# Kernel optimization log

Hardware: AMD Instinct MI355X
Metric: run time of the kernel (lower is better)

The kernel has to match this reference:

```python
import jax, jax.numpy as jnp
import numpy as np

D_MODEL, HEAD, B, S = 1024, 64, 4, 2048

def setup_inputs() -> dict:
    key = jax.random.key(0)
    ks = jax.random.split(key, 7)
    sc = 0.02
    return {
        "x": jax.random.normal(ks[0], (B, S, D_MODEL), dtype=jnp.float32),
        "w_q": jax.random.normal(ks[1], (D_MODEL, HEAD), dtype=jnp.float32) * sc,
        "b_q": jax.random.normal(ks[2], (HEAD,), dtype=jnp.float32) * sc,
        "w_k": jax.random.normal(ks[3], (D_MODEL, HEAD), dtype=jnp.float32) * sc,
        "b_k": jax.random.normal(ks[4], (HEAD,), dtype=jnp.float32) * sc,
        "w_v": jax.random.normal(ks[5], (D_MODEL, HEAD), dtype=jnp.float32) * sc,
        "b_v": jax.random.normal(ks[6], (HEAD,), dtype=jnp.float32) * sc,
    }

def reference(x, w_q, b_q, w_k, b_k, w_v, b_v):
    # q, k, v: [B, S, H]
    q = jnp.einsum('bsd,dh->bsh', x, w_q) + b_q
    k = jnp.einsum('bsd,dh->bsh', x, w_k) + b_k
    v = jnp.einsum('bsd,dh->bsh', x, w_v) + b_v
    head = k.shape[-1]
    # Source divides by (1/sqrt(d)) i.e. multiplies by sqrt(d) -- kept faithful.
    scores = jnp.einsum('bqh,bkh->bqk', q, k) * jnp.sqrt(jnp.float32(head))
    seq = x.shape[1]
    causal = jnp.tril(jnp.ones((seq, seq), dtype=bool))  # [S, S]
    scores = jnp.where(causal, scores, -jnp.inf)
    att = jax.nn.softmax(scores, axis=-1)
    # dropout is identity in eval / p=0
    return jnp.einsum('bqk,bkh->bqh', att, v)
```

## Files before the change

kernel.cpp:

```cpp
#include <hip/hip_runtime.h>
#include <math.h>

#define D_MODEL 1024
#define HEAD 64
#define BATCH 4
#define SEQ 2048
#define M_TOT (BATCH*SEQ)

typedef short short8 __attribute__((ext_vector_type(8)));
typedef float f32x4 __attribute__((ext_vector_type(4)));
typedef unsigned short ushort_t;

__device__ __forceinline__ unsigned short f2bf(float x) {
    union { float f; unsigned u; } v; v.f = x;
    unsigned r = (v.u + 0x7FFFu + ((v.u >> 16) & 1u)) >> 16;
    return (unsigned short)r;
}
__device__ __forceinline__ unsigned short f2bf_trunc(float x) {
    union { float f; unsigned u; } v; v.f = x;
    return (unsigned short)(v.u >> 16);
}
__device__ __forceinline__ float bf2f(unsigned short h) {
    union { unsigned u; float f; } v; v.u = ((unsigned)h) << 16;
    return v.f;
}

__global__ __launch_bounds__(256) void wsplit_kernel(
    const float* __restrict__ wq, const float* __restrict__ wk,
    const float* __restrict__ wv,
    ushort_t* __restrict__ Wfhi, ushort_t* __restrict__ Wflo)
{
    int tid = blockIdx.x * 256 + threadIdx.x;
    int l = tid & 63;
    int c = l & 15, g = l >> 4;
    int rest = tid >> 6;
    int nt = rest % 12, ks = rest / 12;
    const float* W = (nt < 4) ? wq : ((nt < 8) ? wk : wv);
    int colm = ((nt & 3) * 16) + c;
    short8 hi, lo;
#pragma unroll
    for (int e = 0; e < 8; ++e) {
        float v = W[(size_t)(32 * ks + 8 * g + e) * HEAD + colm];
        unsigned short h = f2bf_trunc(v);
        hi[e] = (short)h;
        lo[e] = (short)f2bf(v - bf2f(h));
    }
    *(short8*)&Wfhi[(size_t)tid * 8] = hi;
    *(short8*)&Wflo[(size_t)tid * 8] = lo;
}

#define KSLAB 128
#define XSTR 132

__global__ __launch_bounds__(256) void proj_kernel(
    const float* __restrict__ x,
    const ushort_t* __restrict__ Wfhi, const ushort_t* __restrict__ Wflo,
    const float* __restrict__ bq, const float* __restrict__ bk,
    const float* __restrict__ bv,
    ushort_t* __restrict__ Qhi, ushort_t* __restrict__ Qlo,
    float* __restrict__ Kw, ushort_t* __restrict__ Vt)
{
    __shared__ __align__(16) ushort_t xh_lds[2][16][XSTR];
    __shared__ __align__(16) ushort_t xl_lds[2][16][XSTR];
    __shared__ float eld[4][3][16][17];

    const int t = threadIdx.x;
    const int w = t >> 6;
    const int l = t & 63;
    const int c = l & 15, g = l >> 4;
    const int m0 = blockIdx.x * 16;

    const int st_r = t >> 4;
    const int st_k = (t & 15) * 8;
    const float* xbase = &x[(size_t)(m0 + st_r) * D_MODEL + st_k];

    f32x4 acc[3];
#pragma unroll
    for (int j = 0; j < 3; ++j) acc[j] = (f32x4)0.0f;

    float4 ra, rb;
    {
        const float* xp = xbase;
        ra = *(const float4*)xp;
        rb = *(const float4*)(xp + 4);
    }
    {
        float xs[8] = {ra.x, ra.y, ra.z, ra.w, rb.x, rb.y, rb.z, rb.w};
        short8 hi, lo;
#pragma unroll
        for (int e = 0; e < 8; ++e) {
            unsigned short h = f2bf_trunc(xs[e]);
            hi[e] = (short)h;
            lo[e] = (short)f2bf(xs[e] - bf2f(h));
        }
        *(short8*)&xh_lds[0][st_r][st_k] = hi;
        *(short8*)&xl_lds[0][st_r][st_k] = lo;
    }

#pragma unroll 1
    for (int s = 0; s < 8; ++s) {
        __syncthreads();
        const int buf = s & 1;
        if (s < 7) {
            const float* xp = xbase + (s + 1) * KSLAB;
            ra = *(const float4*)xp;
            rb = *(const float4*)(xp + 4);
        }
#pragma unroll
        for (int ks = 0; ks < 4; ++ks) {
            short8 xh = *(const short8*)&xh_lds[buf][c][ks * 32 + 8 * g];
            short8 xl = *(const short8*)&xl_lds[buf][c][ks * 32 + 8 * g];
            const size_t kg = (size_t)(s * 4 + ks) * 6144;
#pragma unroll
            for (int j = 0; j < 3; ++j) {
                const size_t wo = kg + (size_t)((3 * w + j) * 64 + l) * 8;
                short8 wh = *(const short8*)&Wfhi[wo];
                short8 wl_ = *(const short8*)&Wflo[wo];
                acc[j] = __builtin_amdgcn_mfma_f32_16x16x32_bf16(xh, wh, acc[j], 0, 0, 0);
                acc[j] = __builtin_amdgcn_mfma_f32_16x16x32_bf16(xl, wh, acc[j], 0, 0, 0);
                acc[j] = __builtin_amdgcn_mfma_f32_16x16x32_bf16(xh, wl_, acc[j], 0, 0, 0);
            }
        }
        if (s < 7) {
            float xs[8] = {ra.x, ra.y, ra.z, ra.w, rb.x, rb.y, rb.z, rb.w};
            short8 hi, lo;
#pragma unroll
            for (int e = 0; e < 8; ++e) {
                unsigned short h = f2bf_trunc(xs[e]);
                hi[e] = (short)h;
                lo[e] = (short)f2bf(xs[e] - bf2f(h));
            }
            *(short8*)&xh_lds[buf ^ 1][st_r][st_k] = hi;
            *(short8*)&xl_lds[buf ^ 1][st_r][st_k] = lo;
        }
    }

#pragma unroll
    for (int j = 0; j < 3; ++j)
#pragma unroll
        for (int r = 0; r < 4; ++r)
            eld[w][j][4 * g + r][c] = acc[j][r];

    const int b = m0 >> 11;
    const int s0 = m0 & 2047;

#pragma unroll
    for (int j = 0; j < 3; ++j) {
        const int nt = 3 * w + j;
        const int col16 = (nt & 3) * 16;
        if (nt < 4) {
            const int row = l >> 2, cc4 = (l & 3) * 4;
            unsigned hu[2] = {0, 0}, lu[2] = {0, 0};
#pragma unroll
            for (int i = 0; i < 4; ++i) {
                float v = (eld[w][j][row][cc4 + i] + bq[col16 + cc4 + i]) * 8.0f;
                unsigned short h = f2bf_trunc(v);
                unsigned short lo2 = f2bf(v - bf2f(h));
                hu[i >> 1] |= ((unsigned)h) << ((i & 1) * 16);
                lu[i >> 1] |= ((unsigned)lo2) << ((i & 1) * 16);
            }
            size_t off = (size_t)(m0 + row) * HEAD + col16 + cc4;
            *(uint2*)&Qhi[off] = make_uint2(hu[0], hu[1]);
            *(uint2*)&Qlo[off] = make_uint2(lu[0], lu[1]);
        } else if (nt < 8) {
            const int row = l >> 2, cc4 = (l & 3) * 4;
            float4 o;
            o.x = eld[w][j][row][cc4 + 0] + bk[col16 + cc4 + 0];
            o.y = eld[w][j][row][cc4 + 1] + bk[col16 + cc4 + 1];
            o.z = eld[w][j][row][cc4 + 2] + bk[col16 + cc4 + 2];
            o.w = eld[w][j][row][cc4 + 3] + bk[col16 + cc4 + 3];
            *(float4*)&Kw[(size_t)(m0 + row) * HEAD + col16 + cc4] = o;
        } else {
            const int dl = l >> 2, sg = (l & 3) * 4;
            const float bb = bv[col16 + dl];
            unsigned vu[2] = {0, 0};
#pragma unroll
            for (int i = 0; i < 4; ++i) {
                unsigned short v = f2bf(eld[w][j][sg + i][dl] + bb);
                vu[i >> 1] |= ((unsigned)v) << ((i & 1) * 16);
            }
            *(uint2*)&Vt[((size_t)b * HEAD + col16 + dl) * SEQ + s0 + sg] =
                make_uint2(vu[0], vu[1]);
        }
    }
}

#define NW 4
#define CHUNK 16
#define PSTR 72
#define NSEG 4

__global__ __launch_bounds__(256) void attn_part_kernel(
    const ushort_t* __restrict__ Qhi, const ushort_t* __restrict__ Qlo,
    const float* __restrict__ Kw, const ushort_t* __restrict__ Vt,
    float* __restrict__ Pm_ws, float* __restrict__ Pl_ws,
    float* __restrict__ Po_ws)
{
    __shared__ float Po[NW][CHUNK][68];
    __shared__ float Pm[NW][CHUNK];
    __shared__ float Pl[NW][CHUNK];
    __shared__ __align__(16) ushort_t Plds[NW][CHUNK][PSTR];

    const int t = threadIdx.x;
    const int w = t >> 6;
    const int l = t & 63;
    int id = blockIdx.x;
    int seg, base;
    if (id < 128)      { seg = 0; base = 0;   }
    else if (id < 224) { seg = 1; base = 128; }
    else if (id < 288) { seg = 2; base = 224; }
    else               { seg = 3; base = 288; }
    const int chunk = 127 - (id - base);
    const int b = blockIdx.y;
    const int q0 = chunk * CHUNK;

    const int c = l & 15;
    const int g = l >> 4;

    short8 qhi[2], qlo[2];
    {
        const ushort_t* qbase = &Qhi[(size_t)(b * SEQ + q0 + c) * HEAD];
        const ushort_t* qbasel = &Qlo[(size_t)(b * SEQ + q0 + c) * HEAD];
#pragma unroll
        for (int dc = 0; dc < 2; ++dc) {
            qhi[dc] = *(const short8*)&qbase[dc * 32 + 8 * g];
            qlo[dc] = *(const short8*)&qbasel[dc * 32 + 8 * g];
        }
    }

    f32x4 acc[4];
#pragma unroll
    for (int dt = 0; dt < 4; ++dt) acc[dt] = (f32x4)0.0f;
    float mrun = -1e30f, lsum = 0.f;

#pragma unroll 1
    for (int i = 0; i < 2; ++i) {
        const int tl = seg * 8 + w + 4 * i;
        const int c0 = tl * 64;
        if (c0 > q0 + CHUNK - 1) continue;

        int nlive = ((q0 + 15 - c0) >> 4) + 1;
        nlive = nlive > 4 ? 4 : nlive;

        float sc[4][4];
        float tmax = -1e30f;
#pragma unroll
        for (int t4 = 0; t4 < 4; ++t4) {
            if (t4 < nlive) {
                f32x4 st = (f32x4)0.0f;
#pragma unroll
                for (int dc = 0; dc < 2; ++dc) {
                    const float* kp = &Kw[(size_t)(b * SEQ + c0 + 16 * t4 + c) * HEAD + dc * 32 + 8 * g];
                    float4 a = *(const float4*)kp;
                    float4 b2 = *(const float4*)(kp + 4);
                    float ks8[8] = {a.x, a.y, a.z, a.w, b2.x, b2.y, b2.z, b2.w};
                    short8 khi, klo;
#pragma unroll
                    for (int e = 0; e < 8; ++e) {
                        unsigned short h = f2bf(ks8[e]);
                        khi[e] = (short)h;
                        klo[e] = (short)f2bf(ks8[e] - bf2f(h));
                    }
                    st = __builtin_amdgcn_mfma_f32_16x16x32_bf16(khi, qhi[dc], st, 0, 0, 0);
                    st = __builtin_amdgcn_mfma_f32_16x16x32_bf16(khi, qlo[dc], st, 0, 0, 0);
                    st = __builtin_amdgcn_mfma_f32_16x16x32_bf16(klo, qhi[dc], st, 0, 0, 0);
                }
#pragma unroll
                for (int r = 0; r < 4; ++r) {
                    int kv = c0 + 16 * t4 + 4 * g + r;
                    float s = (kv <= q0 + c) ? st[r] : -1e30f;
                    sc[t4][r] = s;
                    tmax = fmaxf(tmax, s);
                }
            } else {
#pragma unroll
                for (int r = 0; r < 4; ++r) sc[t4][r] = -1e30f;
            }
        }
        tmax = fmaxf(tmax, __shfl_xor(tmax, 16));
        tmax = fmaxf(tmax, __shfl_xor(tmax, 32));
        float newm = fmaxf(mrun, tmax);
        float corr = __expf(mrun - newm);
        mrun = newm;

        float psum = 0.f;
#pragma unroll
        for (int t4 = 0; t4 < 4; ++t4) {
            if (t4 < nlive) {
#pragma unroll
                for (int r = 0; r < 4; ++r) {
                    float pp = __expf(sc[t4][r] - newm);
                    sc[t4][r] = pp;
                    psum += pp;
                }
            } else {
#pragma unroll
                for (int r = 0; r < 4; ++r) sc[t4][r] = 0.f;
            }
        }
        psum += __shfl_xor(psum, 16);
        psum += __shfl_xor(psum, 32);
        lsum = lsum * corr + psum;

#pragma unroll
        for (int r = 0; r < 4; ++r) {
            float cq = __shfl(corr, 4 * g + r);
#pragma unroll
            for (int dt = 0; dt < 4; ++dt) acc[dt][r] *= cq;
        }

#pragma unroll
        for (int t4 = 0; t4 < 4; ++t4) {
            uint2 u;
            u.x = (unsigned)f2bf(sc[t4][0]) | ((unsigned)f2bf(sc[t4][1]) << 16);
            u.y = (unsigned)f2bf(sc[t4][2]) | ((unsigned)f2bf(sc[t4][3]) << 16);
            *(uint2*)&Plds[w][c][16 * t4 + 4 * g] = u;
        }
        const int nkvc = (nlive + 1) >> 1;
#pragma unroll
        for (int kvc = 0; kvc < 2; ++kvc) {
            if (kvc < nkvc) {
                short8 pf = *(short8*)&Plds[w][c][kvc * 32 + 8 * g];
#pragma unroll
                for (int dt = 0; dt < 4; ++dt) {
                    const ushort_t* vp =
                        &Vt[((size_t)(b * HEAD) + 16 * dt + c) * SEQ + c0 + kvc * 32 + 8 * g];
                    short8 vf = *(const short8*)vp;
                    acc[dt] = __builtin_amdgcn_mfma_f32_16x16x32_bf16(pf, vf, acc[dt], 0, 0, 0);
                }
            }
        }
    }

    if (g == 0) { Pm[w][c] = mrun; Pl[w][c] = lsum; }
#pragma unroll
    for (int dt = 0; dt < 4; ++dt)
#pragma unroll
        for (int r = 0; r < 4; ++r)
            Po[w][4 * g + r][16 * dt + c] = acc[dt][r];
    __syncthreads();

    const int mr = t >> 4;
    const int md = (t & 15) * 4;
    float M = Pm[0][mr];
#pragma unroll
    for (int ww = 1; ww < NW; ++ww) M = fmaxf(M, Pm[ww][mr]);
    float L = 0.f;
    float4 O; O.x = O.y = O.z = O.w = 0.f;
#pragma unroll
    for (int ww = 0; ww < NW; ++ww) {
        float f = __expf(Pm[ww][mr] - M);
        L += f * Pl[ww][mr];
        float4 p = *(const float4*)&Po[ww][mr][md];
        O.x += f * p.x; O.y += f * p.y; O.z += f * p.z; O.w += f * p.w;
    }
    const size_t part = ((size_t)(b * 128 + chunk)) * NSEG + seg;
    *(float4*)&Po_ws[(part * CHUNK + mr) * HEAD + md] = O;
    if ((t & 15) == 0) {
        Pm_ws[part * CHUNK + mr] = M;
        Pl_ws[part * CHUNK + mr] = L;
    }
}

__global__ __launch_bounds__(256) void attn_merge_kernel(
    const float* __restrict__ Pm_ws, const float* __restrict__ Pl_ws,
    const float* __restrict__ Po_ws, float* __restrict__ out)
{
    const int t = threadIdx.x;
    const int chunk = blockIdx.x;
    const int b = blockIdx.y;
    const int nparts = (chunk >> 5) + 1;
    const int mr = t >> 4;
    const int md = (t & 15) * 4;
    const size_t pbase = ((size_t)(b * 128 + chunk)) * NSEG;

    float M = -1e30f;
#pragma unroll 1
    for (int p = 0; p < nparts; ++p)
        M = fmaxf(M, Pm_ws[(pbase + p) * CHUNK + mr]);
    float L = 0.f;
    float4 O; O.x = O.y = O.z = O.w = 0.f;
#pragma unroll 1
    for (int p = 0; p < nparts; ++p) {
        float f = __expf(Pm_ws[(pbase + p) * CHUNK + mr] - M);
        L += f * Pl_ws[(pbase + p) * CHUNK + mr];
        float4 po = *(const float4*)&Po_ws[((pbase + p) * CHUNK + mr) * HEAD + md];
        O.x += f * po.x; O.y += f * po.y; O.z += f * po.z; O.w += f * po.w;
    }
    float inv = 1.0f / L;
    float4 res; res.x = O.x * inv; res.y = O.y * inv; res.z = O.z * inv; res.w = O.w * inv;
    *(float4*)&out[(size_t)(b * SEQ + chunk * CHUNK + mr) * HEAD + md] = res;
}

extern "C" void kernel_launch(void* const* d_in, const int* in_sizes, int n_in,
                              void* d_out, int out_size, void* d_ws, size_t ws_size,
                              hipStream_t stream) {
    (void)in_sizes; (void)n_in; (void)out_size; (void)ws_size;
    const float* x  = (const float*)d_in[0];
    const float* wq = (const float*)d_in[1];
    const float* bq = (const float*)d_in[2];
    const float* wk = (const float*)d_in[3];
    const float* bk = (const float*)d_in[4];
    const float* wv = (const float*)d_in[5];
    const float* bv = (const float*)d_in[6];
    float* out = (float*)d_out;

    ushort_t* Wfhi = (ushort_t*)d_ws;
    ushort_t* Wflo = Wfhi + (size_t)D_MODEL * 192;
    ushort_t* Qhi  = Wflo + (size_t)D_MODEL * 192;
    ushort_t* Qlo  = Qhi + (size_t)M_TOT * HEAD;
    float*    Kw   = (float*)(Qlo + (size_t)M_TOT * HEAD);
    ushort_t* Vt   = (ushort_t*)(Kw + (size_t)M_TOT * HEAD);
    float* Pm_ws = (float*)(Vt + (size_t)M_TOT * HEAD);
    float* Pl_ws = Pm_ws + (size_t)BATCH * 128 * NSEG * CHUNK;
    float* Po_ws = Pl_ws + (size_t)BATCH * 128 * NSEG * CHUNK;

    hipLaunchKernelGGL(wsplit_kernel, dim3(96), dim3(256), 0, stream,
                       wq, wk, wv, Wfhi, Wflo);
    hipLaunchKernelGGL(proj_kernel, dim3(M_TOT / 16), dim3(256), 0, stream,
                       x, Wfhi, Wflo, bq, bk, bv, Qhi, Qlo, Kw, Vt);
    hipLaunchKernelGGL(attn_part_kernel, dim3(320, BATCH), dim3(256),
                       0, stream, Qhi, Qlo, Kw, Vt, Pm_ws, Pl_ws, Po_ws);
    hipLaunchKernelGGL(attn_merge_kernel, dim3(SEQ / CHUNK, BATCH), dim3(256),
                       0, stream, Pm_ws, Pl_ws, Po_ws, out);
}
```

Baseline: 81.95 us.

## Stream x and weight slabs directly into LDS with per-wave async double buffering

```diff
diff --git a/kernel.cpp b/kernel.cpp
--- a/kernel.cpp
+++ b/kernel.cpp
@@ -10,6 +10,10 @@
 typedef short short8 __attribute__((ext_vector_type(8)));
 typedef float f32x4 __attribute__((ext_vector_type(4)));
 typedef unsigned short ushort_t;
+
+typedef const __attribute__((address_space(1))) char* gas_t;
+typedef __attribute__((address_space(3))) char* las_t;
+#define GLDS16(src, dst) __builtin_amdgcn_global_load_lds((gas_t)(const void*)(src), (las_t)(void*)(dst), 16, 0, 0)
 
 __device__ __forceinline__ unsigned short f2bf(float x) {
     union { float f; unsigned u; } v; v.f = x;
@@ -49,9 +53,6 @@
     *(short8*)&Wflo[(size_t)tid * 8] = lo;
 }
 
-#define KSLAB 128
-#define XSTR 132
-
 __global__ __launch_bounds__(256) void proj_kernel(
     const float* __restrict__ x,
     const ushort_t* __restrict__ Wfhi, const ushort_t* __restrict__ Wflo,
@@ -60,9 +61,7 @@
     ushort_t* __restrict__ Qhi, ushort_t* __restrict__ Qlo,
     float* __restrict__ Kw, ushort_t* __restrict__ Vt)
 {
-    __shared__ __align__(16) ushort_t xh_lds[2][16][XSTR];
-    __shared__ __align__(16) ushort_t xl_lds[2][16][XSTR];
-    __shared__ float eld[4][3][16][17];
+    __shared__ __align__(16) char pbuf[65536];
 
     const int t = threadIdx.x;
     const int w = t >> 6;
@@ -70,76 +69,65 @@
     const int c = l & 15, g = l >> 4;
     const int m0 = blockIdx.x * 16;
 
-    const int st_r = t >> 4;
-    const int st_k = (t & 15) * 8;
-    const float* xbase = &x[(size_t)(m0 + st_r) * D_MODEL + st_k];
+    char* wbase = pbuf + w * 16384;
 
     f32x4 acc[3];
 #pragma unroll
     for (int j = 0; j < 3; ++j) acc[j] = (f32x4)0.0f;
 
-    float4 ra, rb;
-    {
-        const float* xp = xbase;
-        ra = *(const float4*)xp;
-        rb = *(const float4*)(xp + 4);
-    }
-    {
-        float xs[8] = {ra.x, ra.y, ra.z, ra.w, rb.x, rb.y, rb.z, rb.w};
-        short8 hi, lo;
+    const float* xsrc = &x[(size_t)(m0 + c) * D_MODEL + 8 * g];
+
+#define STAGE(i)                                                              \
+    do {                                                                      \
+        char* sb = wbase + ((i) & 1) * 8192;                                  \
+        const float* xa = xsrc + (i) * 32;                                    \
+        GLDS16(xa, sb);                                                       \
+        GLDS16(xa + 4, sb + 1024);                                            \
+        _Pragma("unroll")                                                     \
+        for (int j = 0; j < 3; ++j) {                                         \
+            const size_t wo = ((size_t)(i) * 12 + 3 * w + j) * 512 + l * 8;   \
+            GLDS16(&Wfhi[wo], sb + 2048 + j * 1024);                          \
+            GLDS16(&Wflo[wo], sb + 5120 + j * 1024);                          \
+        }                                                                     \
+    } while (0)
+
+    STAGE(0);
+    STAGE(1);
+
+#pragma unroll 1
+    for (int i = 0; i < 32; ++i) {
+        if (i < 31) asm volatile("s_waitcnt vmcnt(8)" ::: "memory");
+        else        asm volatile("s_waitcnt vmcnt(0)" ::: "memory");
+        __builtin_amdgcn_sched_barrier(0);
+        char* sb = wbase + (i & 1) * 8192;
+        float4 fa = *(const float4*)(sb + l * 16);
+        float4 fb = *(const float4*)(sb + 1024 + l * 16);
+        float xs8[8] = {fa.x, fa.y, fa.z, fa.w, fb.x, fb.y, fb.z, fb.w};
+        short8 xh, xl;
 #pragma unroll
         for (int e = 0; e < 8; ++e) {
-            unsigned short h = f2bf_trunc(xs[e]);
-            hi[e] = (short)h;
-            lo[e] = (short)f2bf(xs[e] - bf2f(h));
-        }
-        *(short8*)&xh_lds[0][st_r][st_k] = hi;
-        *(short8*)&xl_lds[0][st_r][st_k] = lo;
-    }
-
-#pragma unroll 1
-    for (int s = 0; s < 8; ++s) {
-        __syncthreads();
-        const int buf = s & 1;
-        if (s < 7) {
-            const float* xp = xbase + (s + 1) * KSLAB;
-            ra = *(const float4*)xp;
-            rb = *(const float4*)(xp + 4);
-        }
-#pragma unroll
-        for (int ks = 0; ks < 4; ++ks) {
-            short8 xh = *(const short8*)&xh_lds[buf][c][ks * 32 + 8 * g];
-            short8 xl = *(const short8*)&xl_lds[buf][c][ks * 32 + 8 * g];
-            const size_t kg = (size_t)(s * 4 + ks) * 6144;
-#pragma unroll
-            for (int j = 0; j < 3; ++j) {
-                const size_t wo = kg + (size_t)((3 * w + j) * 64 + l) * 8;
-                short8 wh = *(const short8*)&Wfhi[wo];
-                short8 wl_ = *(const short8*)&Wflo[wo];
-                acc[j] = __builtin_amdgcn_mfma_f32_16x16x32_bf16(xh, wh, acc[j], 0, 0, 0);
-                acc[j] = __builtin_amdgcn_mfma_f32_16x16x32_bf16(xl, wh, acc[j], 0, 0, 0);
-                acc[j] = __builtin_amdgcn_mfma_f32_16x16x32_bf16(xh, wl_, acc[j], 0, 0, 0);
-            }
-        }
-        if (s < 7) {
-            float xs[8] = {ra.x, ra.y, ra.z, ra.w, rb.x, rb.y, rb.z, rb.w};
-            short8 hi, lo;
-#pragma unroll
-            for (int e = 0; e < 8; ++e) {
-                unsigned short h = f2bf_trunc(xs[e]);
-                hi[e] = (short)h;
-                lo[e] = (short)f2bf(xs[e] - bf2f(h));
-            }
-            *(short8*)&xh_lds[buf ^ 1][st_r][st_k] = hi;
-            *(short8*)&xl_lds[buf ^ 1][st_r][st_k] = lo;
-        }
-    }
-
+            unsigned short h = f2bf_trunc(xs8[e]);
+            xh[e] = (short)h;
+            xl[e] = (short)f2bf(xs8[e] - bf2f(h));
+        }
+#pragma unroll
+        for (int j = 0; j < 3; ++j) {
+            short8 wh = *(const short8*)(sb + 2048 + j * 1024 + l * 16);
+            short8 wl_ = *(const short8*)(sb + 5120 + j * 1024 + l * 16);
+            acc[j] = __builtin_amdgcn_mfma_f32_16x16x32_bf16(xh, wh, acc[j], 0, 0, 0);
+            acc[j] = __builtin_amdgcn_mfma_f32_16x16x32_bf16(xl, wh, acc[j], 0, 0, 0);
+            acc[j] = __builtin_amdgcn_mfma_f32_16x16x32_bf16(xh, wl_, acc[j], 0, 0, 0);
+        }
+        if (i < 30) STAGE(i + 2);
+    }
+
+    float* eldw = (float*)wbase;
+#define ELD(j, r, cc) eldw[((j) * 16 + (r)) * 17 + (cc)]
 #pragma unroll
     for (int j = 0; j < 3; ++j)
 #pragma unroll
         for (int r = 0; r < 4; ++r)
-            eld[w][j][4 * g + r][c] = acc[j][r];
+            ELD(j, 4 * g + r, c) = acc[j][r];
 
     const int b = m0 >> 11;
     const int s0 = m0 & 2047;
@@ -153,7 +141,7 @@
             unsigned hu[2] = {0, 0}, lu[2] = {0, 0};
 #pragma unroll
             for (int i = 0; i < 4; ++i) {
-                float v = (eld[w][j][row][cc4 + i] + bq[col16 + cc4 + i]) * 8.0f;
+                float v = (ELD(j, row, cc4 + i) + bq[col16 + cc4 + i]) * 8.0f;
                 unsigned short h = f2bf_trunc(v);
                 unsigned short lo2 = f2bf(v - bf2f(h));
                 hu[i >> 1] |= ((unsigned)h) << ((i & 1) * 16);
@@ -165,10 +153,10 @@
         } else if (nt < 8) {
             const int row = l >> 2, cc4 = (l & 3) * 4;
             float4 o;
-            o.x = eld[w][j][row][cc4 + 0] + bk[col16 + cc4 + 0];
-            o.y = eld[w][j][row][cc4 + 1] + bk[col16 + cc4 + 1];
-            o.z = eld[w][j][row][cc4 + 2] + bk[col16 + cc4 + 2];
-            o.w = eld[w][j][row][cc4 + 3] + bk[col16 + cc4 + 3];
+            o.x = ELD(j, row, cc4 + 0) + bk[col16 + cc4 + 0];
+            o.y = ELD(j, row, cc4 + 1) + bk[col16 + cc4 + 1];
+            o.z = ELD(j, row, cc4 + 2) + bk[col16 + cc4 + 2];
+            o.w = ELD(j, row, cc4 + 3) + bk[col16 + cc4 + 3];
             *(float4*)&Kw[(size_t)(m0 + row) * HEAD + col16 + cc4] = o;
         } else {
             const int dl = l >> 2, sg = (l & 3) * 4;
@@ -176,13 +164,15 @@
             unsigned vu[2] = {0, 0};
 #pragma unroll
             for (int i = 0; i < 4; ++i) {
-                unsigned short v = f2bf(eld[w][j][sg + i][dl] + bb);
+                unsigned short v = f2bf(ELD(j, sg + i, dl) + bb);
                 vu[i >> 1] |= ((unsigned)v) << ((i & 1) * 16);
             }
             *(uint2*)&Vt[((size_t)b * HEAD + col16 + dl) * SEQ + s0 + sg] =
                 make_uint2(vu[0], vu[1]);
         }
     }
+#undef ELD
+#undef STAGE
 }
 
 #define NW 4
```

Measured after the change: 77.07 us, median of 4. -6.0%, faster.
